# Kernel optimization log

Measured on AMD Instinct MI355X. Metric: run time of the kernel, lower is better.

Reference implementation:

```python
import jax, jax.numpy as jnp
import numpy as np
jax.config.update('jax_enable_x64', True)

LAYER_ID = 0
HASH_SEED = 17
N_GRAM_LIST = [2, 3]
NUM_HEADS = 4
HASH_MODULUS = 1023  # engram_vocab_size - 1
HIDDEN = 768
HEAD_DIM = 96
CONV_K = 3
EPS = 1e-6


def _hash_params(n):
    max_int = (1 << 31) - 1
    mults, offs = [], []
    for h in range(NUM_HEADS):
        base = HASH_SEED + 10007 * (LAYER_ID + 1) + 1543 * (n + 1) + 8191 * (h + 1)
        row = []
        for p in range(n):
            v = (base + 32771 * (p + 1) + 65537 * (h + 1) * (p + 1)) % max_int
            row.append(v * 2 + 1)
        mults.append(row)
        offs.append((base * 2147483647 + 97 * (n + h + 1)) % max_int)
    return np.array(mults, dtype=np.int64), np.array(offs, dtype=np.int64)


def _compute_hash_ids(input_ids):
    # input_ids: [B, S] int64 -> hash_ids [B, S, total_heads]
    B, S = input_ids.shape
    parts = []
    for n in N_GRAM_LIST:
        mult_np, off_np = _hash_params(n)
        mult = jnp.asarray(mult_np)  # [H, n]
        off = jnp.asarray(off_np)    # [H]
        # sliding windows of size n: [B, S-n+1, n]
        win = jnp.stack([input_ids[:, p:S - n + 1 + p] for p in range(n)], axis=-1)
        mix = win[:, :, 0, None] * mult[None, None, :, 0]
        for p in range(1, n):
            mix = jnp.bitwise_xor(mix, win[:, :, p, None] * mult[None, None, :, p])
        h = jnp.remainder(mix + off[None, None, :], HASH_MODULUS) + 1  # [B, S-n+1, H]
        h = jnp.pad(h, ((0, 0), (n - 1, 0), (0, 0)))  # first n-1 positions get padding idx 0
        parts.append(h)
    return jnp.concatenate(parts, axis=-1)  # [B, S, 8]


def _rmsnorm(x, w):
    xf = x.astype(jnp.float32)
    var = jnp.mean(xf * xf, axis=-1, keepdims=True)
    return w * (xf * jax.lax.rsqrt(var + EPS)).astype(x.dtype)


def setup_inputs() -> dict:
    key = jax.random.key(0)
    ks = jax.random.split(key, 7)
    B, S = 4, 8192
    hidden_states = jax.random.normal(ks[0], (B, S, HIDDEN), dtype=jnp.float32)
    input_ids = jax.random.randint(ks[1], (B, S), 0, 10240, dtype=jnp.int64)
    emb = 0.02 * jax.random.normal(ks[2], (8, 1024, HEAD_DIM), dtype=jnp.float32)
    emb = emb.at[:, 0, :].set(0.0)  # padding_idx=0
    w_key = 0.02 * jax.random.normal(ks[3], (HIDDEN, HIDDEN), dtype=jnp.float32)
    w_value = 0.02 * jax.random.normal(ks[4], (HIDDEN, HIDDEN), dtype=jnp.float32)
    key_norm_w = jnp.ones((HIDDEN,), dtype=jnp.float32)
    value_norm_w = jnp.ones((HIDDEN,), dtype=jnp.float32)
    conv_w = 0.1 * jax.random.normal(ks[5], (HIDDEN, CONV_K), dtype=jnp.float32)
    return {'hidden_states': hidden_states, 'input_ids': input_ids, 'emb': emb,
            'w_key': w_key, 'w_value': w_value, 'key_norm_w': key_norm_w,
            'value_norm_w': value_norm_w, 'conv_w': conv_w}


def reference(hidden_states, input_ids, emb, w_key, w_value, key_norm_w, value_norm_w, conv_w):
    B, S, H = hidden_states.shape
    hash_ids = _compute_hash_ids(input_ids)  # [B, S, 8]
    # multi-head embedding gather + padding mask + concat -> [B, S, memory_dim]
    heads = jnp.arange(8)[None, None, :]
    gathered = emb[heads, hash_ids]                       # [B, S, 8, head_dim]
    gathered = gathered * (hash_ids != 0)[..., None]      # padding_idx semantics
    memory = gathered.reshape(B, S, 8 * HEAD_DIM)
    memory_key = _rmsnorm(jnp.einsum('bsm,hm->bsh', memory, w_key), key_norm_w)
    memory_value = _rmsnorm(jnp.einsum('bsm,hm->bsh', memory, w_value), value_norm_w)
    gate = jax.nn.sigmoid(jnp.sum(hidden_states * memory_key, axis=-1) / jnp.sqrt(jnp.float32(H)))
    gated = gate[..., None] * memory_value                # [B, S, H]
    # causal depthwise conv1d, kernel size K, left-padded by K-1
    xpad = jnp.pad(gated, ((0, 0), (CONV_K - 1, 0), (0, 0)))
    conv_out = sum(xpad[:, k:k + S, :] * conv_w[:, k][None, None, :] for k in range(CONV_K))
    return conv_out
```

## Files before the change

kernel.cpp:

```cpp
#include <hip/hip_runtime.h>
#include <hip/hip_bf16.h>
#include <stdint.h>

#define B_ 4
#define S_ 8192
#define HID 768
#define NTOK (B_ * S_)

typedef unsigned short u16;
typedef __bf16 bf16x8 __attribute__((ext_vector_type(8)));
typedef float f32x4 __attribute__((ext_vector_type(4)));

struct HashP {
  unsigned long long mult[8][3];
  unsigned long long off[8];
};

static HashP make_hashp() {
  HashP hp;
  const long long max_int = 2147483647LL;
  int gi = 0;
  const int ngrams[2] = {2, 3};
  for (int t = 0; t < 2; ++t) {
    int n = ngrams[t];
    for (int h = 0; h < 4; ++h) {
      long long base = 17 + 10007 * 1 + 1543 * (n + 1) + 8191 * (h + 1);
      for (int p = 0; p < 3; ++p) hp.mult[gi][p] = 0ull;
      for (int p = 0; p < n; ++p) {
        long long v = (base + 32771LL * (p + 1) + 65537LL * (h + 1) * (p + 1)) % max_int;
        hp.mult[gi][p] = (unsigned long long)(v * 2 + 1);
      }
      hp.off[gi] = (unsigned long long)(((base * max_int) + 97LL * (n + h + 1)) % max_int);
      ++gi;
    }
  }
  return hp;
}

__device__ __forceinline__ float b2f(u16 u) {
  union { unsigned int i; float f; } c;
  c.i = ((unsigned int)u) << 16;
  return c.f;
}
__device__ __forceinline__ u16 f2b(float f) {
  union { float f; unsigned int i; } c;
  c.f = f;
  unsigned int r = c.i + 0x7fffu + ((c.i >> 16) & 1u);
  return (u16)(r >> 16);
}

__device__ __forceinline__ void store8b(u16* p, const float* f) {
  uint4 u;
  u.x = (unsigned)f2b(f[0]) | ((unsigned)f2b(f[1]) << 16);
  u.y = (unsigned)f2b(f[2]) | ((unsigned)f2b(f[3]) << 16);
  u.z = (unsigned)f2b(f[4]) | ((unsigned)f2b(f[5]) << 16);
  u.w = (unsigned)f2b(f[6]) | ((unsigned)f2b(f[7]) << 16);
  *reinterpret_cast<uint4*>(p) = u;
}
struct F8 { float f[8]; };
__device__ __forceinline__ F8 load8b(const u16* p) {
  uint4 u = *reinterpret_cast<const uint4*>(p);
  F8 r;
  r.f[0] = b2f((u16)(u.x & 0xffffu)); r.f[1] = b2f((u16)(u.x >> 16));
  r.f[2] = b2f((u16)(u.y & 0xffffu)); r.f[3] = b2f((u16)(u.y >> 16));
  r.f[4] = b2f((u16)(u.z & 0xffffu)); r.f[5] = b2f((u16)(u.z >> 16));
  r.f[6] = b2f((u16)(u.w & 0xffffu)); r.f[7] = b2f((u16)(u.w >> 16));
  return r;
}

__device__ __forceinline__ void gl_lds16(const void* g, void* l) {
  auto gp = reinterpret_cast<const __attribute__((address_space(1))) void*>(
      reinterpret_cast<uintptr_t>(g));
  auto lp = reinterpret_cast<__attribute__((address_space(3))) void*>(
      reinterpret_cast<uintptr_t>(l));
  __builtin_amdgcn_global_load_lds(gp, lp, 16, 0, 0);
}

__global__ __launch_bounds__(256) void k_w2b(
    const float* __restrict__ wk, const float* __restrict__ wv,
    u16* __restrict__ wkb, u16* __restrict__ wvb) {
  int t = blockIdx.x * 256 + threadIdx.x;
  const float* src;
  u16* dst;
  int off;
  if (t < 73728) { src = wk; dst = wkb; off = t * 8; }
  else           { src = wv; dst = wvb; off = (t - 73728) * 8; }
  float4 a = *reinterpret_cast<const float4*>(src + off);
  float4 b = *reinterpret_cast<const float4*>(src + off + 4);
  float f[8] = {a.x, a.y, a.z, a.w, b.x, b.y, b.z, b.w};
  store8b(dst + off, f);
}

__global__ __launch_bounds__(256) void k_hash_gather(
    const int* __restrict__ ids, const float* __restrict__ emb,
    u16* __restrict__ mem, HashP hp) {
  int tid = blockIdx.x * 256 + threadIdx.x;
  int token = tid / 96;
  int j = tid - token * 96;
  if (token >= NTOK) return;
  int b = token >> 13;
  int s = token & (S_ - 1);
  int g = j / 12;
  int d0 = (j - g * 12) * 8;
  int n = (g < 4) ? 2 : 3;
  float f[8] = {0.f, 0.f, 0.f, 0.f, 0.f, 0.f, 0.f, 0.f};
  if (s >= n - 1) {
    const int* row = ids + b * S_;
    unsigned long long mix = 0ull;
    for (int p = 0; p < n; ++p)
      mix ^= (unsigned long long)(unsigned int)row[s - n + 1 + p] * hp.mult[g][p];
    unsigned long long id = (mix + hp.off[g]) % 1023ull + 1ull;
    const float* e = emb + ((size_t)g * 1024 + id) * 96 + d0;
    float4 a = *reinterpret_cast<const float4*>(e);
    float4 c = *reinterpret_cast<const float4*>(e + 4);
    f[0] = a.x; f[1] = a.y; f[2] = a.z; f[3] = a.w;
    f[4] = c.x; f[5] = c.y; f[6] = c.z; f[7] = c.w;
  }
  store8b(mem + (size_t)token * 768 + (size_t)j * 8, f);
}

__global__ __launch_bounds__(256) void k_gemm(
    const u16* __restrict__ A, const u16* __restrict__ Wk,
    const u16* __restrict__ Wv, u16* __restrict__ KV) {
  __shared__ u16 As[128 * 32];
  __shared__ u16 Bs[128 * 32];

  int L = blockIdx.x;
  int xcd = L & 7;
  int idx = L >> 3;
  int mtl = idx / 12;
  int nt = idx - mtl * 12;
  int mt = xcd * 32 + mtl;
  const int m0 = mt * 128;
  const u16* Wbase = (nt < 6) ? (Wk + (size_t)nt * 128 * 768)
                              : (Wv + (size_t)(nt - 6) * 128 * 768);
  const int colbase = nt * 128;

  const int tid = threadIdx.x;
  const int lane = tid & 63;
  const int wv = tid >> 6;
  const int wr = (wv >> 1) * 64;
  const int wc = (wv & 1) * 64;
  const int m16 = lane & 15;
  const int g8 = (lane >> 4) * 8;

  f32x4 acc[4][4];
#pragma unroll
  for (int i = 0; i < 4; ++i)
#pragma unroll
    for (int j = 0; j < 4; ++j) acc[i][j] = (f32x4){0.f, 0.f, 0.f, 0.f};

  for (int kt = 0; kt < 24; ++kt) {
    const int k0 = kt * 32;
#pragma unroll
    for (int i = 0; i < 2; ++i) {
      int c = tid + i * 256;
      int row = c >> 2;
      int kk = (c & 3) * 8;
      gl_lds16(A + (size_t)(m0 + row) * 768 + k0 + kk, &As[c * 8]);
      gl_lds16(Wbase + (size_t)row * 768 + k0 + kk, &Bs[c * 8]);
    }
    __syncthreads();
    bf16x8 af[4], bfr[4];
#pragma unroll
    for (int mi = 0; mi < 4; ++mi)
      af[mi] = *reinterpret_cast<const bf16x8*>(&As[(wr + mi * 16 + m16) * 32 + g8]);
#pragma unroll
    for (int ni = 0; ni < 4; ++ni)
      bfr[ni] = *reinterpret_cast<const bf16x8*>(&Bs[(wc + ni * 16 + m16) * 32 + g8]);
#pragma unroll
    for (int mi = 0; mi < 4; ++mi)
#pragma unroll
      for (int ni = 0; ni < 4; ++ni)
        acc[mi][ni] = __builtin_amdgcn_mfma_f32_16x16x32_bf16(af[mi], bfr[ni],
                                                              acc[mi][ni], 0, 0, 0);
    __syncthreads();
  }

  const int r0 = (lane >> 4) * 4;
#pragma unroll
  for (int mi = 0; mi < 4; ++mi) {
#pragma unroll
    for (int r = 0; r < 4; ++r) {
      int row = m0 + wr + mi * 16 + r0 + r;
      size_t base = (size_t)row * 1536 + colbase + wc;
#pragma unroll
      for (int ni = 0; ni < 4; ++ni)
        KV[base + ni * 16 + m16] = f2b(acc[mi][ni][r]);
    }
  }
}

__global__ __launch_bounds__(256) void k_epi(
    const u16* __restrict__ KV, const float* __restrict__ hid,
    const float* __restrict__ knw, const float* __restrict__ vnw,
    u16* __restrict__ gated) {
  int token = blockIdx.x * 4 + (threadIdx.x >> 6);
  int lane = threadIdx.x & 63;
  const int c0 = lane * 12;
  const u16* kr = KV + (size_t)token * 1536 + c0;
  const u16* vr = kr + 768;
  const float* hr = hid + (size_t)token * 768 + c0;

  float k[12], v[12], h[12];
#pragma unroll
  for (int q = 0; q < 3; ++q) {
    ushort4 a = *reinterpret_cast<const ushort4*>(kr + q * 4);
    ushort4 b = *reinterpret_cast<const ushort4*>(vr + q * 4);
    float4 c = *reinterpret_cast<const float4*>(hr + q * 4);
    k[q * 4 + 0] = b2f(a.x); k[q * 4 + 1] = b2f(a.y);
    k[q * 4 + 2] = b2f(a.z); k[q * 4 + 3] = b2f(a.w);
    v[q * 4 + 0] = b2f(b.x); v[q * 4 + 1] = b2f(b.y);
    v[q * 4 + 2] = b2f(b.z); v[q * 4 + 3] = b2f(b.w);
    h[q * 4 + 0] = c.x; h[q * 4 + 1] = c.y;
    h[q * 4 + 2] = c.z; h[q * 4 + 3] = c.w;
  }
  float ssk = 0.f, ssv = 0.f;
#pragma unroll
  for (int i = 0; i < 12; ++i) { ssk += k[i] * k[i]; ssv += v[i] * v[i]; }
#pragma unroll
  for (int off = 1; off < 64; off <<= 1) {
    ssk += __shfl_xor(ssk, off);
    ssv += __shfl_xor(ssv, off);
  }
  float rk = rsqrtf(ssk * (1.f / 768.f) + 1e-6f);
  float rv = rsqrtf(ssv * (1.f / 768.f) + 1e-6f);

  float dot = 0.f;
#pragma unroll
  for (int i = 0; i < 12; ++i) dot += h[i] * (k[i] * rk * knw[c0 + i]);
#pragma unroll
  for (int off = 1; off < 64; off <<= 1) dot += __shfl_xor(dot, off);
  float gate = 1.f / (1.f + expf(-dot * 0.03608439182435161f));

  float o[12];
#pragma unroll
  for (int i = 0; i < 12; ++i) o[i] = gate * v[i] * rv * vnw[c0 + i];

  u16* go = gated + (size_t)token * 768 + c0;
#pragma unroll
  for (int q = 0; q < 3; ++q) {
    ushort4 u;
    u.x = f2b(o[q * 4 + 0]); u.y = f2b(o[q * 4 + 1]);
    u.z = f2b(o[q * 4 + 2]); u.w = f2b(o[q * 4 + 3]);
    *reinterpret_cast<ushort4*>(go + q * 4) = u;
  }
}

__global__ __launch_bounds__(256) void k_conv(
    const u16* __restrict__ g, const float* __restrict__ cw,
    float* __restrict__ out) {
  int tid = blockIdx.x * 256 + threadIdx.x;
  int token = tid / 96;
  int j = tid - token * 96;
  if (token >= NTOK) return;
  int s = token & (S_ - 1);
  int c0 = j * 8;

  float w[8][3];
#pragma unroll
  for (int i = 0; i < 8; ++i)
#pragma unroll
    for (int kk = 0; kk < 3; ++kk) w[i][kk] = cw[(c0 + i) * 3 + kk];

  float acc[8] = {0.f, 0.f, 0.f, 0.f, 0.f, 0.f, 0.f, 0.f};
#pragma unroll
  for (int kk = 0; kk < 3; ++kk) {
    int d = kk - 2;
    if (s + d < 0) continue;
    F8 x = load8b(g + (size_t)(token + d) * 768 + c0);
#pragma unroll
    for (int i = 0; i < 8; ++i) acc[i] += x.f[i] * w[i][kk];
  }
  float* op = out + (size_t)token * 768 + c0;
  *reinterpret_cast<float4*>(op) = make_float4(acc[0], acc[1], acc[2], acc[3]);
  *reinterpret_cast<float4*>(op + 4) = make_float4(acc[4], acc[5], acc[6], acc[7]);
}

extern "C" void kernel_launch(void* const* d_in, const int* in_sizes, int n_in,
                              void* d_out, int out_size, void* d_ws, size_t ws_size,
                              hipStream_t stream) {
  const float* hid = (const float*)d_in[0];
  const int* ids = (const int*)d_in[1];
  const float* emb = (const float*)d_in[2];
  const float* wk  = (const float*)d_in[3];
  const float* wvw = (const float*)d_in[4];
  const float* knw = (const float*)d_in[5];
  const float* vnw = (const float*)d_in[6];
  const float* cw  = (const float*)d_in[7];
  float* out = (float*)d_out;

  char* ws = (char*)d_ws;
  u16* mem = (u16*)ws;
  u16* kv  = (u16*)(ws + 50331648);
  u16* wkb = (u16*)(ws + 150994944);
  u16* wvb = (u16*)(ws + 152174592);
  u16* gated = mem;

  HashP hp = make_hashp();

  k_w2b<<<576, 256, 0, stream>>>(wk, wvw, wkb, wvb);
  k_hash_gather<<<12288, 256, 0, stream>>>(ids, emb, mem, hp);
  k_gemm<<<3072, 256, 0, stream>>>(mem, wkb, wvb, kv);
  k_epi<<<8192, 256, 0, stream>>>(kv, hid, knw, vnw, gated);
  k_conv<<<12288, 256, 0, stream>>>(gated, cw, out);
}
```

Baseline: 382.9 us.

## Fuse gating epilogue and causal conv into one kernel via shared memory

Merges the RMSNorm/gate epilogue and the depthwise causal conv into a single kernel. Each block computes gated values for 32 tokens plus a 2-token halo into LDS, then applies the 3-tap conv from LDS and writes the output. This removes the global write and re-read of the bf16 gated tensor and one kernel launch. In exchange, each block recomputes 2 halo tokens, the grid is smaller, and LDS use per block goes up.

```diff
diff --git a/kernel.cpp b/kernel.cpp
--- a/kernel.cpp
+++ b/kernel.cpp
@@ -191,90 +191,100 @@
   }
 }
 
-__global__ __launch_bounds__(256) void k_epi(
+#define T_TOK 32
+#define LROW 776
+__global__ __launch_bounds__(256) void k_epiconv(
     const u16* __restrict__ KV, const float* __restrict__ hid,
     const float* __restrict__ knw, const float* __restrict__ vnw,
-    u16* __restrict__ gated) {
-  int token = blockIdx.x * 4 + (threadIdx.x >> 6);
-  int lane = threadIdx.x & 63;
+    const float* __restrict__ cw, float* __restrict__ out) {
+  __shared__ u16 gl[(T_TOK + 2) * LROW];
+
+  const int t0 = blockIdx.x * T_TOK;
+  const int s0 = t0 & (S_ - 1);
+  const int w = threadIdx.x >> 6;
+  const int lane = threadIdx.x & 63;
   const int c0 = lane * 12;
-  const u16* kr = KV + (size_t)token * 1536 + c0;
-  const u16* vr = kr + 768;
-  const float* hr = hid + (size_t)token * 768 + c0;
-
-  float k[12], v[12], h[12];
-#pragma unroll
-  for (int q = 0; q < 3; ++q) {
-    ushort4 a = *reinterpret_cast<const ushort4*>(kr + q * 4);
-    ushort4 b = *reinterpret_cast<const ushort4*>(vr + q * 4);
-    float4 c = *reinterpret_cast<const float4*>(hr + q * 4);
-    k[q * 4 + 0] = b2f(a.x); k[q * 4 + 1] = b2f(a.y);
-    k[q * 4 + 2] = b2f(a.z); k[q * 4 + 3] = b2f(a.w);
-    v[q * 4 + 0] = b2f(b.x); v[q * 4 + 1] = b2f(b.y);
-    v[q * 4 + 2] = b2f(b.z); v[q * 4 + 3] = b2f(b.w);
-    h[q * 4 + 0] = c.x; h[q * 4 + 1] = c.y;
-    h[q * 4 + 2] = c.z; h[q * 4 + 3] = c.w;
-  }
-  float ssk = 0.f, ssv = 0.f;
-#pragma unroll
-  for (int i = 0; i < 12; ++i) { ssk += k[i] * k[i]; ssv += v[i] * v[i]; }
-#pragma unroll
-  for (int off = 1; off < 64; off <<= 1) {
-    ssk += __shfl_xor(ssk, off);
-    ssv += __shfl_xor(ssv, off);
-  }
-  float rk = rsqrtf(ssk * (1.f / 768.f) + 1e-6f);
-  float rv = rsqrtf(ssv * (1.f / 768.f) + 1e-6f);
-
-  float dot = 0.f;
-#pragma unroll
-  for (int i = 0; i < 12; ++i) dot += h[i] * (k[i] * rk * knw[c0 + i]);
-#pragma unroll
-  for (int off = 1; off < 64; off <<= 1) dot += __shfl_xor(dot, off);
-  float gate = 1.f / (1.f + expf(-dot * 0.03608439182435161f));
-
-  float o[12];
-#pragma unroll
-  for (int i = 0; i < 12; ++i) o[i] = gate * v[i] * rv * vnw[c0 + i];
-
-  u16* go = gated + (size_t)token * 768 + c0;
-#pragma unroll
-  for (int q = 0; q < 3; ++q) {
-    ushort4 u;
-    u.x = f2b(o[q * 4 + 0]); u.y = f2b(o[q * 4 + 1]);
-    u.z = f2b(o[q * 4 + 2]); u.w = f2b(o[q * 4 + 3]);
-    *reinterpret_cast<ushort4*>(go + q * 4) = u;
-  }
-}
-
-__global__ __launch_bounds__(256) void k_conv(
-    const u16* __restrict__ g, const float* __restrict__ cw,
-    float* __restrict__ out) {
-  int tid = blockIdx.x * 256 + threadIdx.x;
-  int token = tid / 96;
-  int j = tid - token * 96;
-  if (token >= NTOK) return;
-  int s = token & (S_ - 1);
-  int c0 = j * 8;
-
-  float w[8][3];
-#pragma unroll
-  for (int i = 0; i < 8; ++i)
-#pragma unroll
-    for (int kk = 0; kk < 3; ++kk) w[i][kk] = cw[(c0 + i) * 3 + kk];
-
-  float acc[8] = {0.f, 0.f, 0.f, 0.f, 0.f, 0.f, 0.f, 0.f};
-#pragma unroll
-  for (int kk = 0; kk < 3; ++kk) {
-    int d = kk - 2;
-    if (s + d < 0) continue;
-    F8 x = load8b(g + (size_t)(token + d) * 768 + c0);
-#pragma unroll
-    for (int i = 0; i < 8; ++i) acc[i] += x.f[i] * w[i][kk];
-  }
-  float* op = out + (size_t)token * 768 + c0;
-  *reinterpret_cast<float4*>(op) = make_float4(acc[0], acc[1], acc[2], acc[3]);
-  *reinterpret_cast<float4*>(op + 4) = make_float4(acc[4], acc[5], acc[6], acc[7]);
+
+  for (int j = w; j < T_TOK + 2; j += 4) {
+    if (!(s0 == 0 && j < 2)) {
+      const int token = t0 + j - 2;
+      const u16* kr = KV + (size_t)token * 1536 + c0;
+      const u16* vr = kr + 768;
+      const float* hr = hid + (size_t)token * 768 + c0;
+
+      float k[12], v[12], h[12];
+#pragma unroll
+      for (int q = 0; q < 3; ++q) {
+        ushort4 a = *reinterpret_cast<const ushort4*>(kr + q * 4);
+        ushort4 b = *reinterpret_cast<const ushort4*>(vr + q * 4);
+        float4 c = *reinterpret_cast<const float4*>(hr + q * 4);
+        k[q * 4 + 0] = b2f(a.x); k[q * 4 + 1] = b2f(a.y);
+        k[q * 4 + 2] = b2f(a.z); k[q * 4 + 3] = b2f(a.w);
+        v[q * 4 + 0] = b2f(b.x); v[q * 4 + 1] = b2f(b.y);
+        v[q * 4 + 2] = b2f(b.z); v[q * 4 + 3] = b2f(b.w);
+        h[q * 4 + 0] = c.x; h[q * 4 + 1] = c.y;
+        h[q * 4 + 2] = c.z; h[q * 4 + 3] = c.w;
+      }
+      float ssk = 0.f, ssv = 0.f;
+#pragma unroll
+      for (int i = 0; i < 12; ++i) { ssk += k[i] * k[i]; ssv += v[i] * v[i]; }
+#pragma unroll
+      for (int off = 1; off < 64; off <<= 1) {
+        ssk += __shfl_xor(ssk, off);
+        ssv += __shfl_xor(ssv, off);
+      }
+      float rk = rsqrtf(ssk * (1.f / 768.f) + 1e-6f);
+      float rv = rsqrtf(ssv * (1.f / 768.f) + 1e-6f);
+
+      float dot = 0.f;
+#pragma unroll
+      for (int i = 0; i < 12; ++i) dot += h[i] * (k[i] * rk * knw[c0 + i]);
+#pragma unroll
+      for (int off = 1; off < 64; off <<= 1) dot += __shfl_xor(dot, off);
+      float gate = 1.f / (1.f + expf(-dot * 0.03608439182435161f));
+
+      u16* go = &gl[j * LROW + c0];
+#pragma unroll
+      for (int q = 0; q < 3; ++q) {
+        ushort4 u;
+        u.x = f2b(gate * v[q * 4 + 0] * rv * vnw[c0 + q * 4 + 0]);
+        u.y = f2b(gate * v[q * 4 + 1] * rv * vnw[c0 + q * 4 + 1]);
+        u.z = f2b(gate * v[q * 4 + 2] * rv * vnw[c0 + q * 4 + 2]);
+        u.w = f2b(gate * v[q * 4 + 3] * rv * vnw[c0 + q * 4 + 3]);
+        *reinterpret_cast<ushort4*>(go + q * 4) = u;
+      }
+    }
+  }
+  __syncthreads();
+
+#pragma unroll
+  for (int it = 0; it < 12; ++it) {
+    int job = threadIdx.x + it * 256;
+    int r = job / 96;
+    int cg = job - r * 96;
+    int cc0 = cg * 8;
+    int s = s0 + r;
+
+    float acc[8] = {0.f, 0.f, 0.f, 0.f, 0.f, 0.f, 0.f, 0.f};
+    if (s >= 2) {
+      F8 x0 = load8b(&gl[r * LROW + cc0]);
+#pragma unroll
+      for (int i = 0; i < 8; ++i) acc[i] += x0.f[i] * cw[(cc0 + i) * 3 + 0];
+    }
+    if (s >= 1) {
+      F8 x1 = load8b(&gl[(r + 1) * LROW + cc0]);
+#pragma unroll
+      for (int i = 0; i < 8; ++i) acc[i] += x1.f[i] * cw[(cc0 + i) * 3 + 1];
+    }
+    {
+      F8 x2 = load8b(&gl[(r + 2) * LROW + cc0]);
+#pragma unroll
+      for (int i = 0; i < 8; ++i) acc[i] += x2.f[i] * cw[(cc0 + i) * 3 + 2];
+    }
+    float* op = out + (size_t)(t0 + r) * 768 + cc0;
+    *reinterpret_cast<float4*>(op) = make_float4(acc[0], acc[1], acc[2], acc[3]);
+    *reinterpret_cast<float4*>(op + 4) = make_float4(acc[4], acc[5], acc[6], acc[7]);
+  }
 }
 
 extern "C" void kernel_launch(void* const* d_in, const int* in_sizes, int n_in,
@@ -295,13 +305,11 @@
   u16* kv  = (u16*)(ws + 50331648);
   u16* wkb = (u16*)(ws + 150994944);
   u16* wvb = (u16*)(ws + 152174592);
-  u16* gated = mem;
 
   HashP hp = make_hashp();
 
   k_w2b<<<576, 256, 0, stream>>>(wk, wvw, wkb, wvb);
   k_hash_gather<<<12288, 256, 0, stream>>>(ids, emb, mem, hp);
   k_gemm<<<3072, 256, 0, stream>>>(mem, wkb, wvb, kv);
-  k_epi<<<8192, 256, 0, stream>>>(kv, hid, knw, vnw, gated);
-  k_conv<<<12288, 256, 0, stream>>>(gated, cw, out);
-}
+  k_epiconv<<<1024, 256, 0, stream>>>(kv, hid, knw, vnw, cw, out);
+}
```

Result: faster. 346.4 us (-9.5%).
